# Performance work log

Hardware: AMD Instinct MI355X
Metric: run time of the kernel (lower is better)

Reference implementation:

```python
import jax, jax.numpy as jnp
import numpy as np

N, K, DIM = 65536, 32, 64


def setup_inputs() -> dict:
    key = jax.random.key(0)
    k1, k2, k3, k4 = jax.random.split(key, 4)
    x = jax.random.normal(k1, (N, DIM), jnp.float32)
    log_pi = jax.random.normal(k2, (K, 1), jnp.float32)
    mu = jax.random.normal(k3, (K, DIM), jnp.float32)
    log_sigma_ = jax.random.normal(k4, (K, DIM, DIM), jnp.float32) / 100.0
    return {"x": x, "log_pi": log_pi, "mu": mu, "log_sigma_": log_sigma_}


def reference(x, log_pi, mu, log_sigma_):
    k, d = mu.shape
    # Faithful to torch: softmax over the size-1 last axis of (K,1) -> all ones.
    pi = jax.nn.softmax(log_pi, axis=-1)  # (K, 1)
    # scale_tril construction: strict lower triangle kept, diagonal -> exp(diag) + 1e-3
    diag = jnp.exp(jnp.diagonal(log_sigma_, axis1=-2, axis2=-1)) + 1e-3  # (K, d)
    L = jnp.tril(log_sigma_, -1) + jnp.eye(d, dtype=x.dtype) * diag[:, None, :]  # (K, d, d)
    # batched MVN log_prob via triangular solve
    diff = x[:, None, :] - mu[None, :, :]            # (N, K, d)
    b = jnp.transpose(diff, (1, 2, 0))               # (K, d, N)
    z = jax.scipy.linalg.solve_triangular(L, b, lower=True)  # (K, d, N)
    maha = jnp.sum(z * z, axis=1)                    # (K, N)
    logdet = jnp.sum(jnp.log(diag), axis=-1)         # (K,)
    logp = -0.5 * (maha + d * jnp.log(2.0 * jnp.pi)) - logdet[:, None]  # (K, N)
    p = jnp.exp(logp).T                              # (N, K)
    return jnp.log(jnp.matmul(p, pi).squeeze())      # (N,)
```

## Files before the change

### kernel.cpp

```cpp
#include <hip/hip_runtime.h>

#define KK 32
#define DD 64
#define NB 65536
#define PAD 68
#define FRAGS 6
#define SLOT (FRAGS * 64)
#define MREF 103.0f

typedef __attribute__((ext_vector_type(8))) short bf16x8;
typedef __attribute__((ext_vector_type(4))) float f32x4;

__device__ inline short f2bf(float f) {
  uint32_t u = __builtin_bit_cast(uint32_t, f);
  uint32_t r = (u + 0x7fffu + ((u >> 16) & 1u)) >> 16;
  return (short)(r & 0xffffu);
}
__device__ inline float bf2f(short h) {
  uint32_t u = ((uint32_t)(unsigned short)h) << 16;
  return __builtin_bit_cast(float, u);
}
__device__ inline uint4 pack8(const short* v) {
  uint4 u;
  u.x = (uint32_t)(unsigned short)v[0] | ((uint32_t)(unsigned short)v[1] << 16);
  u.y = (uint32_t)(unsigned short)v[2] | ((uint32_t)(unsigned short)v[3] << 16);
  u.z = (uint32_t)(unsigned short)v[4] | ((uint32_t)(unsigned short)v[5] << 16);
  u.w = (uint32_t)(unsigned short)v[6] | ((uint32_t)(unsigned short)v[7] << 16);
  return u;
}

__device__ __forceinline__ void gl_lds16(const uint4* g, uint4* l) {
  __builtin_amdgcn_global_load_lds(
      (__attribute__((address_space(1))) void*)g,
      (__attribute__((address_space(3))) void*)l, 16, 0, 0);
}

__global__ __launch_bounds__(256) void md_prep(const float* __restrict__ ls,
                                               const float* __restrict__ mu,
                                               uint4* __restrict__ Bp,
                                               float* __restrict__ Cc,
                                               float* __restrict__ Kc2) {
  __shared__ float Ls[DD * DD];
  __shared__ float Ys[DD * PAD];
  __shared__ float invdL[DD];
  __shared__ float muL[DD];
  const int k = blockIdx.x, t = threadIdx.x;
  const int j = t >> 2, sub = t & 3;
  const float* __restrict__ lsk = ls + (size_t)k * DD * DD;

#pragma unroll
  for (int it = 0; it < 4; ++it) {
    const int o = (it * 256 + t) * 4;
    *(float4*)&Ls[o] = *(const float4*)&lsk[o];
  }
  if (t < DD) muL[t] = mu[k * DD + t];
  __syncthreads();
  if (t < DD) invdL[t] = 1.0f / (expf(Ls[t * DD + t]) + 1e-3f);
  __syncthreads();

  const float invdj = invdL[j];
  float z[16];
#pragma unroll
  for (int mi = 0; mi < 16; ++mi) z[mi] = 0.f;
#pragma unroll
  for (int i = 0; i < DD; ++i) {
    float p = 0.f;
#pragma unroll
    for (int mi = 0; mi < 16; ++mi) {
      if (4 * mi < i) {
        const int m = 4 * mi + sub;
        p = fmaf(Ls[i * DD + m], (m < i) ? z[mi] : 0.f, p);
      }
    }
    p += __shfl_xor(p, 1, 64);
    p += __shfl_xor(p, 2, 64);
    const float zi = (i == j) ? invdj : -p * invdL[i];
    if (sub == (i & 3)) z[i >> 2] = zi;
  }
#pragma unroll
  for (int mi = 0; mi < 16; ++mi) Ys[(4 * mi + sub) * PAD + j] = z[mi];
  __syncthreads();

  {
    float p = 0.f;
#pragma unroll
    for (int mi = 0; mi < 16; ++mi) {
      const int m = 4 * mi + sub;
      p = fmaf(Ys[j * PAD + m], muL[m], p);
    }
    p += __shfl_xor(p, 1, 64);
    p += __shfl_xor(p, 2, 64);
    if (sub == 0) Cc[k * DD + j] = p;
  }

  if (t < DD) {
    float r = -logf(invdL[t]);
#pragma unroll
    for (int off = 32; off > 0; off >>= 1) r += __shfl_down(r, off, 64);
    if (t == 0) Kc2[k] = MREF - 0.5f * (64.0f * 1.83787706640934534f) - r;
  }

  if (t < DD) {
    const int colp = t & 15, qp = t >> 4;
    uint4* slot = Bp + (size_t)k * SLOT;
#pragma unroll
    for (int s = 0; s < 2; ++s) {
#pragma unroll
      for (int ct = 0; ct < 4; ++ct) {
        if (s == 1 && ct < 2) continue;
        const int i = colp + 16 * ct;
        const float4 v0 = *(const float4*)&Ys[i * PAD + s * 32 + qp * 8];
        const float4 v1 = *(const float4*)&Ys[i * PAD + s * 32 + qp * 8 + 4];
        const float f[8] = {v0.x, v0.y, v0.z, v0.w, v1.x, v1.y, v1.z, v1.w};
        short hh[8];
#pragma unroll
        for (int jj = 0; jj < 8; ++jj) hh[jj] = f2bf(f[jj]);
        const int fi = (s == 0) ? ct : (2 + ct);
        slot[fi * 64 + t] = pack8(hh);
      }
    }
  }
}

__global__ __launch_bounds__(256, 2) void md_main(const float* __restrict__ x,
                                                  const uint4* __restrict__ Bp,
                                                  const float* __restrict__ Cc,
                                                  const float* __restrict__ Kc2,
                                                  float* __restrict__ P) {
  __shared__ uint4 lds4[2 * SLOT];
  const int tid = threadIdx.x, lane = tid & 63, w = tid >> 6;
  const int quarter = blockIdx.x & 3;
  const int sblk = blockIdx.x >> 2;
  const int base = sblk * 256 + w * 64;
  const int k0 = quarter * 8;
  const int col = lane & 15, q = lane >> 4;

  bf16x8 Xh[4][2], Xl[4][2];
#pragma unroll
  for (int Bt = 0; Bt < 4; ++Bt) {
#pragma unroll
    for (int s = 0; s < 2; ++s) {
      const float* src = x + (size_t)(base + Bt * 16 + col) * DD + s * 32 + q * 8;
      const float4 v0 = *(const float4*)src;
      const float4 v1 = *(const float4*)(src + 4);
      const float f[8] = {v0.x, v0.y, v0.z, v0.w, v1.x, v1.y, v1.z, v1.w};
      bf16x8 h, l;
#pragma unroll
      for (int jj = 0; jj < 8; ++jj) {
        const short hb = f2bf(f[jj]);
        h[jj] = hb;
        l[jj] = f2bf(f[jj] - bf2f(hb));
      }
      Xh[Bt][s] = h;
      Xl[Bt][s] = l;
    }
  }

  const int nfr = (w < 2) ? 2 : 1;
  const int fr0 = (w < 2) ? 2 * w : (2 + w);

  {
    const uint4* src = Bp + (size_t)k0 * SLOT;
#pragma unroll
    for (int it = 0; it < 2; ++it)
      if (it < nfr)
        gl_lds16(src + (fr0 + it) * 64 + lane, &lds4[(fr0 + it) * 64]);
  }
  __syncthreads();

  float run_s[4] = {0.f, 0.f, 0.f, 0.f};

#pragma unroll
  for (int kk = 0; kk < 8; ++kk) {
    const int k = k0 + kk;
    const int p = kk & 1;
    if (kk < 7) {
      const uint4* src = Bp + (size_t)(k + 1) * SLOT;
#pragma unroll
      for (int it = 0; it < 2; ++it)
        if (it < nfr)
          gl_lds16(src + (fr0 + it) * 64 + lane,
                   &lds4[(1 - p) * SLOT + (fr0 + it) * 64]);
    }
    const float kc = Kc2[k];

    const uint4* buf = &lds4[p * SLOT];
    f32x4 mah[4];
#pragma unroll
    for (int Bt = 0; Bt < 4; ++Bt) mah[Bt] = (f32x4){0.f, 0.f, 0.f, 0.f};

#pragma unroll
    for (int ct = 0; ct < 4; ++ct) {
      const bf16x8 A0 = *(const bf16x8*)&buf[ct * 64 + lane];
      bf16x8 A1{};
      if (ct >= 2) A1 = *(const bf16x8*)&buf[(2 + ct) * 64 + lane];
      const f32x4 ci = -*(const f32x4*)&Cc[k * DD + ct * 16 + q * 4];
#pragma unroll
      for (int Bt = 0; Bt < 4; ++Bt) {
        f32x4 z1 = ci;
        z1 = __builtin_amdgcn_mfma_f32_16x16x32_bf16(A0, Xh[Bt][0], z1, 0, 0, 0);
        z1 = __builtin_amdgcn_mfma_f32_16x16x32_bf16(A0, Xl[Bt][0], z1, 0, 0, 0);
        if (ct >= 2) {
          f32x4 z2 = (f32x4){0.f, 0.f, 0.f, 0.f};
          z2 = __builtin_amdgcn_mfma_f32_16x16x32_bf16(A1, Xh[Bt][1], z2, 0, 0, 0);
          z2 = __builtin_amdgcn_mfma_f32_16x16x32_bf16(A1, Xl[Bt][1], z2, 0, 0, 0);
          z1 += z2;
        }
        mah[Bt] += z1 * z1;
      }
    }

#pragma unroll
    for (int Bt = 0; Bt < 4; ++Bt) {
      float s = (mah[Bt][0] + mah[Bt][1]) + (mah[Bt][2] + mah[Bt][3]);
      s += __shfl_xor(s, 16, 64);
      s += __shfl_xor(s, 32, 64);
      const float tt = fmaf(-0.5f, s, kc);
      run_s[Bt] += __expf(tt);
    }

    if (kk < 7) __syncthreads();
  }

  if (q == 0) {
#pragma unroll
    for (int Bt = 0; Bt < 4; ++Bt) {
      const int sid = base + Bt * 16 + col;
      P[quarter * NB + sid] = run_s[Bt];
    }
  }
}

__global__ __launch_bounds__(256) void md_comb(const float* __restrict__ P,
                                               float* __restrict__ out) {
  const int n = blockIdx.x * 256 + threadIdx.x;
  const float S = (P[n] + P[NB + n]) + (P[2 * NB + n] + P[3 * NB + n]);
  out[n] = logf(S) - MREF;
}

extern "C" void kernel_launch(void* const* d_in, const int* in_sizes, int n_in,
                              void* d_out, int out_size, void* d_ws, size_t ws_size,
                              hipStream_t stream) {
  const float* x  = (const float*)d_in[0];
  const float* mu = (const float*)d_in[2];
  const float* ls = (const float*)d_in[3];
  float* out = (float*)d_out;

  char* ws = (char*)d_ws;
  uint4* Bp  = (uint4*)ws;
  float* P   = (float*)(ws + (size_t)KK * SLOT * 16);
  float* Cc  = P + 4 * NB;
  float* Kc2 = Cc + KK * DD;

  md_prep<<<KK, 256, 0, stream>>>(ls, mu, Bp, Cc, Kc2);
  md_main<<<1024, 256, 0, stream>>>(x, Bp, Cc, Kc2, P);
  md_comb<<<NB / 256, 256, 0, stream>>>(P, out);
}
```

Measured before the change: 112.4 us.

## Drop bf16 split of x by folding identity into inverse and adding fp32 x

Stores L^{-1} minus the identity in the bf16 operand and seeds the MFMA accumulator with fp32 x. The identity part of z is then computed exactly, so the low-half bf16 split of x and its MFMAs can be dropped. This halves the MFMA count and removes the Xl registers. It also stages the per-block Cc slice in shared memory and uses exp2 with prescaled constants. The extra fp32 x fragment loads add registers and global traffic, and precision now depends on the off-identity part being small.

```diff
diff --git a/kernel.cpp b/kernel.cpp
--- a/kernel.cpp
+++ b/kernel.cpp
@@ -7,6 +7,7 @@
 #define FRAGS 6
 #define SLOT (FRAGS * 64)
 #define MREF 103.0f
+#define L2E 1.4426950408889634f
 
 typedef __attribute__((ext_vector_type(8))) short bf16x8;
 typedef __attribute__((ext_vector_type(4))) float f32x4;
@@ -15,10 +16,6 @@
   uint32_t u = __builtin_bit_cast(uint32_t, f);
   uint32_t r = (u + 0x7fffu + ((u >> 16) & 1u)) >> 16;
   return (short)(r & 0xffffu);
-}
-__device__ inline float bf2f(short h) {
-  uint32_t u = ((uint32_t)(unsigned short)h) << 16;
-  return __builtin_bit_cast(float, u);
 }
 __device__ inline uint4 pack8(const short* v) {
   uint4 u;
@@ -39,7 +36,7 @@
                                                const float* __restrict__ mu,
                                                uint4* __restrict__ Bp,
                                                float* __restrict__ Cc,
-                                               float* __restrict__ Kc2) {
+                                               float* __restrict__ Kcl2) {
   __shared__ float Ls[DD * DD];
   __shared__ float Ys[DD * PAD];
   __shared__ float invdL[DD];
@@ -97,7 +94,8 @@
     float r = -logf(invdL[t]);
 #pragma unroll
     for (int off = 32; off > 0; off >>= 1) r += __shfl_down(r, off, 64);
-    if (t == 0) Kc2[k] = MREF - 0.5f * (64.0f * 1.83787706640934534f) - r;
+    if (t == 0)
+      Kcl2[k] = (MREF - 0.5f * (64.0f * 1.83787706640934534f) - r) * L2E;
   }
 
   if (t < DD) {
@@ -109,12 +107,13 @@
       for (int ct = 0; ct < 4; ++ct) {
         if (s == 1 && ct < 2) continue;
         const int i = colp + 16 * ct;
-        const float4 v0 = *(const float4*)&Ys[i * PAD + s * 32 + qp * 8];
-        const float4 v1 = *(const float4*)&Ys[i * PAD + s * 32 + qp * 8 + 4];
-        const float f[8] = {v0.x, v0.y, v0.z, v0.w, v1.x, v1.y, v1.z, v1.w};
         short hh[8];
 #pragma unroll
-        for (int jj = 0; jj < 8; ++jj) hh[jj] = f2bf(f[jj]);
+        for (int jj = 0; jj < 8; ++jj) {
+          const int m = s * 32 + qp * 8 + jj;
+          const float v = Ys[i * PAD + m] - ((i == m) ? 1.0f : 0.0f);
+          hh[jj] = f2bf(v);
+        }
         const int fi = (s == 0) ? ct : (2 + ct);
         slot[fi * 64 + t] = pack8(hh);
       }
@@ -125,9 +124,10 @@
 __global__ __launch_bounds__(256, 2) void md_main(const float* __restrict__ x,
                                                   const uint4* __restrict__ Bp,
                                                   const float* __restrict__ Cc,
-                                                  const float* __restrict__ Kc2,
+                                                  const float* __restrict__ Kcl2,
                                                   float* __restrict__ P) {
   __shared__ uint4 lds4[2 * SLOT];
+  __shared__ float CcL[8 * DD];
   const int tid = threadIdx.x, lane = tid & 63, w = tid >> 6;
   const int quarter = blockIdx.x & 3;
   const int sblk = blockIdx.x >> 2;
@@ -135,7 +135,7 @@
   const int k0 = quarter * 8;
   const int col = lane & 15, q = lane >> 4;
 
-  bf16x8 Xh[4][2], Xl[4][2];
+  bf16x8 Xh[4][2];
 #pragma unroll
   for (int Bt = 0; Bt < 4; ++Bt) {
 #pragma unroll
@@ -144,17 +144,23 @@
       const float4 v0 = *(const float4*)src;
       const float4 v1 = *(const float4*)(src + 4);
       const float f[8] = {v0.x, v0.y, v0.z, v0.w, v1.x, v1.y, v1.z, v1.w};
-      bf16x8 h, l;
-#pragma unroll
-      for (int jj = 0; jj < 8; ++jj) {
-        const short hb = f2bf(f[jj]);
-        h[jj] = hb;
-        l[jj] = f2bf(f[jj] - bf2f(hb));
-      }
+      bf16x8 h;
+#pragma unroll
+      for (int jj = 0; jj < 8; ++jj) h[jj] = f2bf(f[jj]);
       Xh[Bt][s] = h;
-      Xl[Bt][s] = l;
-    }
-  }
+    }
+  }
+
+  f32x4 xg[4][4];
+#pragma unroll
+  for (int ct = 0; ct < 4; ++ct)
+#pragma unroll
+    for (int Bt = 0; Bt < 4; ++Bt)
+      xg[ct][Bt] = *(const f32x4*)&x[(size_t)(base + Bt * 16 + col) * DD +
+                                     ct * 16 + q * 4];
+
+  CcL[tid] = Cc[k0 * DD + tid];
+  CcL[256 + tid] = Cc[k0 * DD + 256 + tid];
 
   const int nfr = (w < 2) ? 2 : 1;
   const int fr0 = (w < 2) ? 2 * w : (2 + w);
@@ -182,7 +188,7 @@
           gl_lds16(src + (fr0 + it) * 64 + lane,
                    &lds4[(1 - p) * SLOT + (fr0 + it) * 64]);
     }
-    const float kc = Kc2[k];
+    const float kc = Kcl2[k];
 
     const uint4* buf = &lds4[p * SLOT];
     f32x4 mah[4];
@@ -194,19 +200,15 @@
       const bf16x8 A0 = *(const bf16x8*)&buf[ct * 64 + lane];
       bf16x8 A1{};
       if (ct >= 2) A1 = *(const bf16x8*)&buf[(2 + ct) * 64 + lane];
-      const f32x4 ci = -*(const f32x4*)&Cc[k * DD + ct * 16 + q * 4];
+      const f32x4 cK = *(const f32x4*)&CcL[kk * DD + ct * 16 + q * 4];
 #pragma unroll
       for (int Bt = 0; Bt < 4; ++Bt) {
-        f32x4 z1 = ci;
-        z1 = __builtin_amdgcn_mfma_f32_16x16x32_bf16(A0, Xh[Bt][0], z1, 0, 0, 0);
-        z1 = __builtin_amdgcn_mfma_f32_16x16x32_bf16(A0, Xl[Bt][0], z1, 0, 0, 0);
-        if (ct >= 2) {
-          f32x4 z2 = (f32x4){0.f, 0.f, 0.f, 0.f};
-          z2 = __builtin_amdgcn_mfma_f32_16x16x32_bf16(A1, Xh[Bt][1], z2, 0, 0, 0);
-          z2 = __builtin_amdgcn_mfma_f32_16x16x32_bf16(A1, Xl[Bt][1], z2, 0, 0, 0);
-          z1 += z2;
-        }
-        mah[Bt] += z1 * z1;
+        f32x4 z = xg[ct][Bt];
+        z = __builtin_amdgcn_mfma_f32_16x16x32_bf16(A0, Xh[Bt][0], z, 0, 0, 0);
+        if (ct >= 2)
+          z = __builtin_amdgcn_mfma_f32_16x16x32_bf16(A1, Xh[Bt][1], z, 0, 0, 0);
+        const f32x4 d = z - cK;
+        mah[Bt] += d * d;
       }
     }
 
@@ -215,8 +217,8 @@
       float s = (mah[Bt][0] + mah[Bt][1]) + (mah[Bt][2] + mah[Bt][3]);
       s += __shfl_xor(s, 16, 64);
       s += __shfl_xor(s, 32, 64);
-      const float tt = fmaf(-0.5f, s, kc);
-      run_s[Bt] += __expf(tt);
+      const float tt = fmaf(-0.5f * L2E, s, kc);
+      run_s[Bt] += exp2f(tt);
     }
 
     if (kk < 7) __syncthreads();
@@ -247,12 +249,12 @@
   float* out = (float*)d_out;
 
   char* ws = (char*)d_ws;
-  uint4* Bp  = (uint4*)ws;
-  float* P   = (float*)(ws + (size_t)KK * SLOT * 16);
-  float* Cc  = P + 4 * NB;
-  float* Kc2 = Cc + KK * DD;
-
-  md_prep<<<KK, 256, 0, stream>>>(ls, mu, Bp, Cc, Kc2);
-  md_main<<<1024, 256, 0, stream>>>(x, Bp, Cc, Kc2, P);
+  uint4* Bp   = (uint4*)ws;
+  float* P    = (float*)(ws + (size_t)KK * SLOT * 16);
+  float* Cc   = P + 4 * NB;
+  float* Kcl2 = Cc + KK * DD;
+
+  md_prep<<<KK, 256, 0, stream>>>(ls, mu, Bp, Cc, Kcl2);
+  md_main<<<1024, 256, 0, stream>>>(x, Bp, Cc, Kcl2, P);
   md_comb<<<NB / 256, 256, 0, stream>>>(P, out);
 }
```

Result: no change. 111.1 us (-1.2%).
